# Performance work log

Measured on AMD Instinct MI355X. Metric: run time of the kernel, lower is better.

## Reference

```python
import jax, jax.numpy as jnp
import numpy as np

H, W = 32, 64          # img_size
NB = 4                 # fno_blocks
SCALE = 0.02


def setup_inputs() -> dict:
    key = jax.random.key(0)
    ks = jax.random.split(key, 8)
    B, N, C = 16, H * W, 768
    BS = C // NB
    x = jax.random.normal(ks[0], (B, N, C), dtype=jnp.float32)
    w1 = SCALE * jax.random.normal(ks[1], (2, NB, BS, BS), dtype=jnp.float32)
    b1 = SCALE * jax.random.normal(ks[2], (2, NB, BS), dtype=jnp.float32)
    w2 = SCALE * jax.random.normal(ks[3], (2, NB, BS, BS), dtype=jnp.float32)
    b2 = SCALE * jax.random.normal(ks[4], (2, NB, BS), dtype=jnp.float32)
    # Conv1d(C, C, kernel_size=1) == per-token linear layer over channels
    bias_w = jax.random.normal(ks[5], (C, C), dtype=jnp.float32) / np.sqrt(C)
    bias_b = jax.random.normal(ks[6], (C,), dtype=jnp.float32) * 0.01
    return {"x": x, "w1": w1, "b1": b1, "w2": w2, "b2": b2,
            "bias_w": bias_w, "bias_b": bias_b}


def _mul(a, w):
    # block-diagonal matmul: a [..., NB, BS], w [NB, BS, BS]
    return jnp.einsum('...bd,bdk->...bk', a, w)


def reference(x, w1, b1, w2, b2, bias_w, bias_b):
    B, N, C = x.shape
    BS = C // NB
    # Conv1d kernel-size-1 bias path
    bias = x @ bias_w.T + bias_b
    # spatial FFT
    xf = jnp.fft.rfftn(x.reshape(B, H, W, C), axes=(1, 2), norm='ortho')
    xf = xf.reshape(B, H, W // 2 + 1, NB, BS)
    xr, xi = xf.real, xf.imag
    # layer 1 (complex block-diag matmul + bias, ReLU on real/imag separately)
    r1 = jax.nn.relu(_mul(xr, w1[0]) - _mul(xi, w1[1]) + b1[0])
    i1 = jax.nn.relu(_mul(xr, w1[1]) + _mul(xi, w1[0]) + b1[1])
    # layer 2 -- NOTE: imag part uses the *updated* real part, matching the
    # original torch code's in-place reassignment order.
    r2 = _mul(r1, w2[0]) - _mul(i1, w2[1]) + b2[0]
    i2 = _mul(r2, w2[1]) + _mul(i1, w2[0]) + b2[1]
    xc = jax.lax.complex(r2, i2).reshape(B, H, W // 2 + 1, C)
    out = jnp.fft.irfftn(xc, s=(H, W), axes=(1, 2), norm='ortho')
    return out.reshape(B, N, C) + bias
```

## Files before the change

kernel.cpp:

```cpp
#include <hip/hip_runtime.h>
#include <hip/hip_bf16.h>
#include <stdint.h>

#define BB 16
#define HH 32
#define WW 64
#define CC 768
#define W2C 33
#define ROWW (2*CC)

typedef __bf16 bf16x8 __attribute__((ext_vector_type(8)));
typedef float f32x4 __attribute__((ext_vector_type(4)));

__device__ __forceinline__ unsigned short f2bf(float f) {
  __hip_bfloat16 h = __float2bfloat16(f);
  return __builtin_bit_cast(unsigned short, h);
}
__device__ __forceinline__ float bf2f(unsigned short u) {
  union { unsigned int i; float f; } x;
  x.i = ((unsigned int)u) << 16;
  return x.f;
}

__device__ __forceinline__ void g2l16(const void* g, void* l) {
  __builtin_amdgcn_global_load_lds((const __attribute__((address_space(1))) unsigned int*)g,
                                   (__attribute__((address_space(3))) unsigned int*)l,
                                   16, 0, 0);
}

__device__ __host__ constexpr int brevc(int x, int bits) {
  int r = 0;
  for (int i = 0; i < bits; ++i) r |= ((x >> i) & 1) << (bits - 1 - i);
  return r;
}

constexpr double TPI = 6.283185307179586476925286766559;
constexpr double tsin_(double x) {
  double t = x, s = x, x2 = x * x;
  for (int i = 1; i < 14; ++i) { t *= -x2 / (double)((2 * i) * (2 * i + 1)); s += t; }
  return s;
}
constexpr double tcos_(double x) {
  double t = 1.0, s = 1.0, x2 = x * x;
  for (int i = 1; i < 14; ++i) { t *= -x2 / (double)((2 * i - 1) * (2 * i)); s += t; }
  return s;
}
struct Tw64 { float c[64]; float s[64]; };
constexpr Tw64 mk_tw() {
  Tw64 r{};
  for (int k = 0; k < 64; ++k) {
    int q = k >> 4, m = k & 15;
    double a = (TPI / 64.0) * m;
    double cq = tcos_(a), sq = tsin_(a);
    double c, s;
    if (q == 0)      { c =  cq; s =  sq; }
    else if (q == 1) { c = -sq; s =  cq; }
    else if (q == 2) { c = -cq; s = -sq; }
    else             { c =  sq; s = -cq; }
    r.c[k] = (float)c;
    r.s[k] = (float)(-s);
  }
  return r;
}
constexpr Tw64 TW = mk_tw();

template<int N, bool INV>
__device__ __forceinline__ void fft_reg(float2 (&v)[N]) {
  constexpr int LOG2N = (N == 64) ? 6 : 5;
#pragma unroll
  for (int s = 0; s < LOG2N; ++s) {
    const int len = N >> s;
    const int half = len >> 1;
    const int tstep = 64 / len;
#pragma unroll
    for (int i = 0; i < N; i += len) {
#pragma unroll
      for (int j = 0; j < half; ++j) {
        float2 u = v[i + j];
        float2 t = v[i + j + half];
        float sr = u.x + t.x, si = u.y + t.y;
        float dr = u.x - t.x, di = u.y - t.y;
        float wr = TW.c[j * tstep];
        float wi = INV ? -TW.s[j * tstep] : TW.s[j * tstep];
        v[i + j] = make_float2(sr, si);
        v[i + j + half] = make_float2(dr * wr - di * wi, dr * wi + di * wr);
      }
    }
  }
}

__global__ __launch_bounds__(128) void fft_fwd_w(const float* __restrict__ x,
                                                 ushort2* __restrict__ yw,
                                                 unsigned short* __restrict__ xb) {
  __shared__ __align__(16) float xs[32][128];
  const int t = threadIdx.x;
  const int bh = blockIdx.x;
  const int c0 = blockIdx.y * 128;
  const float* xrow = x + (size_t)bh * (WW * CC) + c0;
  unsigned short* xbrow = xb + (size_t)bh * (WW * CC) + c0;
  const int rg = t >> 5;
  const int lc = (t & 31) * 4;
  float2 v[32];
#pragma unroll
  for (int half = 0; half < 2; ++half) {
    if (half) __syncthreads();
#pragma unroll
    for (int it = 0; it < 8; ++it) {
      const int w = half * 32 + it * 4 + rg;
      float4 f = *(const float4*)(xrow + (size_t)w * CC + lc);
      *(float4*)&xs[it * 4 + rg][lc] = f;
      *(ushort4*)(xbrow + (size_t)w * CC + lc) =
          make_ushort4(f2bf(f.x), f2bf(f.y), f2bf(f.z), f2bf(f.w));
    }
    __syncthreads();
#pragma unroll
    for (int n = 0; n < 16; ++n)
      v[half * 16 + n] = make_float2(xs[2 * n][t], xs[2 * n + 1][t]);
  }
  fft_reg<32, false>(v);
  ushort2* yp = yw + (size_t)bh * (W2C * CC) + c0 + t;
  {
    float2 Z0 = v[0];
    yp[0] = make_ushort2(f2bf(Z0.x + Z0.y), f2bf(0.f));
    yp[(size_t)32 * CC] = make_ushort2(f2bf(Z0.x - Z0.y), f2bf(0.f));
  }
#pragma unroll
  for (int k = 1; k < 32; ++k) {
    float2 Zk = v[brevc(k, 5)];
    float2 Zm = v[brevc(32 - k, 5)];
    float Er = 0.5f * (Zk.x + Zm.x), Ei = 0.5f * (Zk.y - Zm.y);
    float Odr = 0.5f * (Zk.y + Zm.y), Odi = -0.5f * (Zk.x - Zm.x);
    float wx = TW.c[k], wy = TW.s[k];
    float Xr = Er + wx * Odr - wy * Odi;
    float Xi = Ei + wx * Odi + wy * Odr;
    yp[(size_t)k * CC] = make_ushort2(f2bf(Xr), f2bf(Xi));
  }
}

__global__ __launch_bounds__(256) void fft_fwd_h(const ushort2* __restrict__ yw,
                                                 unsigned short* __restrict__ xf) {
  const int bk = blockIdx.x;
  const int b = bk / W2C, kw = bk - b * W2C;
  const int c = blockIdx.y * 256 + threadIdx.x;
  const ushort2* yp = yw + ((size_t)b * HH * W2C + kw) * CC + c;
  float2 v[32];
#pragma unroll
  for (int h = 0; h < 32; ++h) {
    ushort2 u = yp[(size_t)h * (W2C * CC)];
    v[h] = make_float2(bf2f(u.x), bf2f(u.y));
  }
  fft_reg<32, false>(v);
  const int nb = c / 192, cc = c - nb * 192;
  unsigned short* xp = xf + (size_t)nb * 384 + cc;
  const float s = 0.022097086912079608f;
#pragma unroll
  for (int kh = 0; kh < 32; ++kh) {
    float2 z = v[brevc(kh, 5)];
    size_t m = ((size_t)b * HH + kh) * W2C + kw;
    xp[m * ROWW] = f2bf(z.x * s);
    xp[m * ROWW + 192] = f2bf(z.y * s);
  }
}

__global__ __launch_bounds__(256) void fft_inv_h(const unsigned short* __restrict__ r2,
                                                 ushort2* __restrict__ g) {
  const int bk = blockIdx.x;
  const int b = bk / W2C, kw = bk - b * W2C;
  const int c = blockIdx.y * 256 + threadIdx.x;
  const int nb = c / 192, cc = c - nb * 192;
  const unsigned short* rp = r2 + (size_t)nb * 384 + cc;
  float2 v[32];
#pragma unroll
  for (int kh = 0; kh < 32; ++kh) {
    size_t m = ((size_t)b * HH + kh) * W2C + kw;
    v[kh] = make_float2(bf2f(rp[m * ROWW]), bf2f(rp[m * ROWW + 192]));
  }
  fft_reg<32, true>(v);
  ushort2* gp = g + ((size_t)b * HH * W2C + kw) * CC + c;
#pragma unroll
  for (int h = 0; h < 32; ++h) {
    float2 z = v[brevc(h, 5)];
    gp[(size_t)h * (W2C * CC)] = make_ushort2(f2bf(z.x), f2bf(z.y));
  }
}

__global__ __launch_bounds__(128) void fft_inv_w(const ushort2* __restrict__ g,
                                                 const unsigned short* __restrict__ biasb,
                                                 float* __restrict__ out) {
  __shared__ __align__(16) float ys[32][128];
  const int t = threadIdx.x;
  const int bh = blockIdx.x;
  const int c0 = blockIdx.y * 128;
  const ushort2* gp = g + (size_t)bh * (W2C * CC) + c0 + t;
  float2 v[32];
  {
    float X0 = bf2f(gp[0].x);
    float X32 = bf2f(gp[(size_t)32 * CC].x);
    v[0] = make_float2(0.5f * (X0 + X32), 0.5f * (X0 - X32));
  }
#pragma unroll
  for (int k = 1; k < 32; ++k) {
    ushort2 uk = gp[(size_t)k * CC];
    ushort2 um = gp[(size_t)(32 - k) * CC];
    float2 Xk = make_float2(bf2f(uk.x), bf2f(uk.y));
    float2 Xm = make_float2(bf2f(um.x), bf2f(um.y));
    float Ar = 0.5f * (Xk.x + Xm.x), Ai = 0.5f * (Xk.y - Xm.y);
    float Dr = 0.5f * (Xk.x - Xm.x), Di = 0.5f * (Xk.y + Xm.y);
    float wx = TW.c[k], wy = TW.s[k];
    float Br = wx * Dr + wy * Di;
    float Bi = wx * Di - wy * Dr;
    v[k] = make_float2(Ar - Bi, Ai + Br);
  }
  fft_reg<32, true>(v);
  const float s2 = 0.04419417382415922f;
  float* orow = out + (size_t)bh * (WW * CC) + c0;
  const unsigned short* brow = biasb + (size_t)bh * (WW * CC) + c0;
  const int rg = t >> 5;
  const int lc = (t & 31) * 4;
#pragma unroll
  for (int half = 0; half < 2; ++half) {
    if (half) __syncthreads();
#pragma unroll
    for (int n = 0; n < 16; ++n) {
      float2 z = v[brevc(half * 16 + n, 5)];
      ys[2 * n][t] = z.x * s2;
      ys[2 * n + 1][t] = z.y * s2;
    }
    __syncthreads();
#pragma unroll
    for (int it = 0; it < 8; ++it) {
      const int w = half * 32 + it * 4 + rg;
      float4 f = *(const float4*)&ys[it * 4 + rg][lc];
      ushort4 b4 = *(const ushort4*)(brow + (size_t)w * CC + lc);
      f.x += bf2f(b4.x); f.y += bf2f(b4.y); f.z += bf2f(b4.z); f.w += bf2f(b4.w);
      *(float4*)(orow + (size_t)w * CC + lc) = f;
    }
  }
}

template<bool RELU, bool OBF>
__global__ __launch_bounds__(256) void gemm_bt(
    const unsigned short* __restrict__ A, int lda, int aZ,
    const unsigned short* __restrict__ Bw, int K, int bZ,
    const float* __restrict__ bias, int biasZ,
    void* __restrict__ outp, int ldo, int oZ) {
  __shared__ __align__(16) unsigned short As[128 * 32];
  __shared__ __align__(16) unsigned short Bs[128 * 32];
  const int t = threadIdx.x;
  const int z = blockIdx.z;
  const size_t m0 = (size_t)blockIdx.x * 128;
  const int n0 = blockIdx.y * 128;
  const unsigned short* Ap = A + m0 * lda + (size_t)z * aZ;
  const unsigned short* Bp = Bw + (size_t)n0 * K + (size_t)z * bZ;
  const int lane = t & 63, wave = t >> 6;
  const int lr = lane & 15, quad = lane >> 4;
  const int wm = (wave >> 1) * 64, wn = (wave & 1) * 64;
  const int row = t >> 2;
  const int sl = t & 3;
  const int kb = (sl ^ ((row >> 1) & 3)) * 8;
  const int swzf = (lr >> 1) & 3;
  f32x4 acc[4][4] = {};
  for (int k0 = 0; k0 < K; k0 += 32) {
    const unsigned short* ga = Ap + (size_t)row * lda + (k0 + kb);
    g2l16(ga, &As[row * 32 + sl * 8]);
    g2l16(ga + (size_t)64 * lda, &As[(row + 64) * 32 + sl * 8]);
    const unsigned short* gb = Bp + (size_t)row * K + (k0 + kb);
    g2l16(gb, &Bs[row * 32 + sl * 8]);
    g2l16(gb + (size_t)64 * K, &Bs[(row + 64) * 32 + sl * 8]);
    __syncthreads();
    bf16x8 af[4], bfr[4];
#pragma unroll
    for (int mi = 0; mi < 4; ++mi)
      af[mi] = *(const bf16x8*)&As[(wm + mi * 16 + lr) * 32 + ((quad ^ swzf) * 8)];
#pragma unroll
    for (int ni = 0; ni < 4; ++ni)
      bfr[ni] = *(const bf16x8*)&Bs[(wn + ni * 16 + lr) * 32 + ((quad ^ swzf) * 8)];
#pragma unroll
    for (int mi = 0; mi < 4; ++mi)
#pragma unroll
      for (int ni = 0; ni < 4; ++ni)
        acc[mi][ni] = __builtin_amdgcn_mfma_f32_16x16x32_bf16(af[mi], bfr[ni], acc[mi][ni], 0, 0, 0);
    __syncthreads();
  }
#pragma unroll
  for (int mi = 0; mi < 4; ++mi) {
    const size_t mrow = m0 + wm + mi * 16 + quad * 4;
#pragma unroll
    for (int ni = 0; ni < 4; ++ni) {
      const int ncol = n0 + wn + ni * 16 + lr;
      const float bv = bias[z * biasZ + ncol];
#pragma unroll
      for (int r = 0; r < 4; ++r) {
        float vv = acc[mi][ni][r] + bv;
        if (RELU) vv = fmaxf(vv, 0.f);
        const size_t off = (mrow + r) * (size_t)ldo + (size_t)z * oZ + ncol;
        if (OBF) ((unsigned short*)outp)[off] = f2bf(vv);
        else ((float*)outp)[off] = vv;
      }
    }
  }
}

__global__ __launch_bounds__(256) void cvt_bf16(const float* __restrict__ in,
                                                unsigned short* __restrict__ outp) {
  const size_t i = ((size_t)blockIdx.x * 256 + threadIdx.x) * 4;
  float4 v = *(const float4*)(in + i);
  ushort4 o = make_ushort4(f2bf(v.x), f2bf(v.y), f2bf(v.z), f2bf(v.w));
  *(ushort4*)(outp + i) = o;
}

__global__ __launch_bounds__(256) void build_w1(const float* __restrict__ w1,
                                                const float* __restrict__ b1,
                                                unsigned short* __restrict__ w1t,
                                                float* __restrict__ bias1) {
  const int idx = blockIdx.x * 256 + threadIdx.x;
  const int nb = idx / (384 * 384);
  const int rem = idx - nb * (384 * 384);
  const int n = rem / 384, k = rem - (rem / 384) * 384;
  const bool khi = k >= 192, nhi = n >= 192;
  const int kk = khi ? k - 192 : k, nn = nhi ? n - 192 : n;
  float val;
  if (!khi && !nhi)      val =  w1[((0 * 4 + nb) * 192 + kk) * 192 + nn];
  else if (khi && !nhi)  val = -w1[((1 * 4 + nb) * 192 + kk) * 192 + nn];
  else if (!khi && nhi)  val =  w1[((1 * 4 + nb) * 192 + kk) * 192 + nn];
  else                   val =  w1[((0 * 4 + nb) * 192 + kk) * 192 + nn];
  w1t[((size_t)nb * 384 + n) * 384 + k] = f2bf(val);
  if (k == 0)
    bias1[nb * 384 + n] = nhi ? b1[(1 * 4 + nb) * 192 + nn] : b1[(0 * 4 + nb) * 192 + nn];
}

__global__ __launch_bounds__(256) void build_w2(const float* __restrict__ w2,
                                                const float* __restrict__ b2,
                                                unsigned short* __restrict__ w2t,
                                                float* __restrict__ bias2) {
  const int idx = blockIdx.x * 256 + threadIdx.x;
  const int nb = idx / (384 * 384);
  const int rem = idx - nb * (384 * 384);
  const int n = rem / 384, k = rem - (rem / 384) * 384;
  const bool khi = k >= 192, nhi = n >= 192;
  const int kk = khi ? k - 192 : k, nn = nhi ? n - 192 : n;
  float val;
  if (!khi && !nhi) {
    val = w2[((0 * 4 + nb) * 192 + kk) * 192 + nn];
  } else if (khi && !nhi) {
    val = -w2[((1 * 4 + nb) * 192 + kk) * 192 + nn];
  } else if (!khi && nhi) {
    float s = 0.f;
    for (int d = 0; d < 192; ++d)
      s += w2[((0 * 4 + nb) * 192 + kk) * 192 + d] * w2[((1 * 4 + nb) * 192 + d) * 192 + nn];
    val = s;
  } else {
    float s = 0.f;
    for (int d = 0; d < 192; ++d)
      s += w2[((1 * 4 + nb) * 192 + kk) * 192 + d] * w2[((1 * 4 + nb) * 192 + d) * 192 + nn];
    val = w2[((0 * 4 + nb) * 192 + kk) * 192 + nn] - s;
  }
  w2t[((size_t)nb * 384 + n) * 384 + k] = f2bf(val);
  if (k == 0) {
    float bv;
    if (!nhi) {
      bv = b2[(0 * 4 + nb) * 192 + nn];
    } else {
      float s = 0.f;
      for (int d = 0; d < 192; ++d)
        s += b2[(0 * 4 + nb) * 192 + d] * w2[((1 * 4 + nb) * 192 + d) * 192 + nn];
      bv = b2[(1 * 4 + nb) * 192 + nn] + s;
    }
    bias2[nb * 384 + n] = bv;
  }
}

extern "C" void kernel_launch(void* const* d_in, const int* in_sizes, int n_in,
                              void* d_out, int out_size, void* d_ws, size_t ws_size,
                              hipStream_t stream) {
  (void)in_sizes; (void)n_in; (void)out_size; (void)ws_size;
  const float* x  = (const float*)d_in[0];
  const float* w1 = (const float*)d_in[1];
  const float* b1 = (const float*)d_in[2];
  const float* w2 = (const float*)d_in[3];
  const float* b2 = (const float*)d_in[4];
  const float* bw = (const float*)d_in[5];
  const float* bb = (const float*)d_in[6];
  float* out = (float*)d_out;

  char* p = (char*)d_ws;
  unsigned short* buf1 = (unsigned short*)p; p += 51904512;
  unsigned short* buf2 = (unsigned short*)p; p += 51904512;
  unsigned short* buf3 = (unsigned short*)p; p += 51904512;
  unsigned short* bwb  = (unsigned short*)p; p += 1179648;
  unsigned short* w1t  = (unsigned short*)p; p += 1179648;
  unsigned short* w2t  = (unsigned short*)p; p += 1179648;
  float* bias1 = (float*)p; p += 6144;
  float* bias2 = (float*)p; p += 6144;

  cvt_bf16<<<589824 / 1024, 256, 0, stream>>>(bw, bwb);
  build_w1<<<589824 / 256, 256, 0, stream>>>(w1, b1, w1t, bias1);
  build_w2<<<589824 / 256, 256, 0, stream>>>(w2, b2, w2t, bias2);
  fft_fwd_w<<<dim3(BB * HH, 6), 128, 0, stream>>>(x, (ushort2*)buf1, buf2);
  fft_fwd_h<<<dim3(BB * W2C, 3), 256, 0, stream>>>((const ushort2*)buf1, buf3);
  gemm_bt<true, true><<<dim3(132, 3, 4), 256, 0, stream>>>(
      buf3, ROWW, 384, w1t, 384, 384 * 384, bias1, 384, buf1, ROWW, 384);
  gemm_bt<false, true><<<dim3(256, 6, 1), 256, 0, stream>>>(
      buf2, 768, 0, bwb, 768, 0, bb, 0, buf3, 768, 0);
  gemm_bt<false, true><<<dim3(132, 3, 4), 256, 0, stream>>>(
      buf1, ROWW, 384, w2t, 384, 384 * 384, bias2, 384, buf2, ROWW, 384);
  fft_inv_h<<<dim3(BB * W2C, 3), 256, 0, stream>>>(buf2, (ushort2*)buf1);
  fft_inv_w<<<dim3(BB * HH, 6), 128, 0, stream>>>((const ushort2*)buf1, buf3, out);
}
```

Before: 470.2 us.

## Pipeline GEMM loads with 4-stage LDS ring and wider bias-GEMM tiles

Replaces the single-buffered GEMM with a 4-stage shared-memory ring. Tiles are prefetched three steps ahead with explicit vmcnt waits and one barrier per k-step, so global loads overlap the MFMA work. It also raises wave priority around the MFMAs. The bias GEMM now uses 512-thread blocks with 128x256 tiles and an L2-friendly block-index swizzle. The cost is more LDS per block (up to 96 KB), which may cut occupancy, and hand-tuned wait counts that are fragile if the load count changes.

```diff
diff --git a/kernel.cpp b/kernel.cpp
--- a/kernel.cpp
+++ b/kernel.cpp
@@ -238,64 +238,89 @@
   }
 }
 
-template<bool RELU, bool OBF>
-__global__ __launch_bounds__(256) void gemm_bt(
+#define WAITVM(n) asm volatile("s_waitcnt vmcnt(" #n ")" ::: "memory")
+#define MEMFENCE() asm volatile("" ::: "memory")
+
+template<int WN, int BROWS, int NT, bool RELU>
+__global__ __launch_bounds__(128 * WN) void gemm_p(
     const unsigned short* __restrict__ A, int lda, int aZ,
-    const unsigned short* __restrict__ Bw, int K, int bZ,
+    const unsigned short* __restrict__ Bw, int ldb, int bZ,
     const float* __restrict__ bias, int biasZ,
-    void* __restrict__ outp, int ldo, int oZ) {
-  __shared__ __align__(16) unsigned short As[128 * 32];
-  __shared__ __align__(16) unsigned short Bs[128 * 32];
+    unsigned short* __restrict__ outp, int ldo, int oZ, int swzq) {
+  constexpr int BLOCK = 128 * WN;
+  constexpr int RPP = BLOCK / 4;
+  constexpr int PA = 128 / RPP;
+  constexpr int PB = BROWS / RPP;
+  constexpr int LT = PA + PB;
+  __shared__ __align__(16) unsigned short As[4][128 * 32];
+  __shared__ __align__(16) unsigned short Bs[4][BROWS * 32];
   const int t = threadIdx.x;
+  int bx = blockIdx.x;
+  if (swzq) bx = (bx & 7) * swzq + (bx >> 3);
   const int z = blockIdx.z;
-  const size_t m0 = (size_t)blockIdx.x * 128;
-  const int n0 = blockIdx.y * 128;
-  const unsigned short* Ap = A + m0 * lda + (size_t)z * aZ;
-  const unsigned short* Bp = Bw + (size_t)n0 * K + (size_t)z * bZ;
+  const size_t m0 = (size_t)bx * 128;
+  const int n0 = blockIdx.y * BROWS;
   const int lane = t & 63, wave = t >> 6;
   const int lr = lane & 15, quad = lane >> 4;
-  const int wm = (wave >> 1) * 64, wn = (wave & 1) * 64;
-  const int row = t >> 2;
-  const int sl = t & 3;
-  const int kb = (sl ^ ((row >> 1) & 3)) * 8;
-  const int swzf = (lr >> 1) & 3;
+  const int wmo = (wave / WN) * 64;
+  const int wno = (wave % WN) * 64;
+  const int srow = t >> 2, sl = t & 3;
+  const int kb = (sl ^ ((srow >> 1) & 3)) * 8;
+  const int coff = ((quad ^ ((lr >> 1) & 3)) * 8);
+  const unsigned short* Abase = A + (size_t)z * aZ + (m0 + srow) * (size_t)lda + kb;
+  const unsigned short* Bbase = Bw + (size_t)z * bZ + (size_t)(n0 + srow) * ldb + kb;
   f32x4 acc[4][4] = {};
-  for (int k0 = 0; k0 < K; k0 += 32) {
-    const unsigned short* ga = Ap + (size_t)row * lda + (k0 + kb);
-    g2l16(ga, &As[row * 32 + sl * 8]);
-    g2l16(ga + (size_t)64 * lda, &As[(row + 64) * 32 + sl * 8]);
-    const unsigned short* gb = Bp + (size_t)row * K + (k0 + kb);
-    g2l16(gb, &Bs[row * 32 + sl * 8]);
-    g2l16(gb + (size_t)64 * K, &Bs[(row + 64) * 32 + sl * 8]);
-    __syncthreads();
-    bf16x8 af[4], bfr[4];
+
+#define STG(tt_) do { \
+    const int s_ = (tt_) & 3; const int k0_ = (tt_) * 32; \
+    _Pragma("unroll") \
+    for (int p = 0; p < PA; ++p) \
+      g2l16(Abase + (size_t)(p * RPP) * lda + k0_, &As[s_][(srow + p * RPP) * 32 + sl * 8]); \
+    _Pragma("unroll") \
+    for (int p = 0; p < PB; ++p) \
+      g2l16(Bbase + (size_t)(p * RPP) * ldb + k0_, &Bs[s_][(srow + p * RPP) * 32 + sl * 8]); \
+  } while (0)
+
+  STG(0); STG(1); STG(2);
+  if constexpr (LT == 3) WAITVM(6); else WAITVM(8);
+  MEMFENCE(); __builtin_amdgcn_s_barrier(); MEMFENCE();
+
+  for (int tt = 0; tt < NT; ++tt) {
+    if (tt < NT - 3) STG(tt + 3);
+    const int s = tt & 3;
+    bf16x8 af[4], bfv[4];
 #pragma unroll
     for (int mi = 0; mi < 4; ++mi)
-      af[mi] = *(const bf16x8*)&As[(wm + mi * 16 + lr) * 32 + ((quad ^ swzf) * 8)];
+      af[mi] = *(const bf16x8*)&As[s][(wmo + mi * 16 + lr) * 32 + coff];
 #pragma unroll
     for (int ni = 0; ni < 4; ++ni)
-      bfr[ni] = *(const bf16x8*)&Bs[(wn + ni * 16 + lr) * 32 + ((quad ^ swzf) * 8)];
+      bfv[ni] = *(const bf16x8*)&Bs[s][(wno + ni * 16 + lr) * 32 + coff];
+    __builtin_amdgcn_s_setprio(1);
 #pragma unroll
     for (int mi = 0; mi < 4; ++mi)
 #pragma unroll
       for (int ni = 0; ni < 4; ++ni)
-        acc[mi][ni] = __builtin_amdgcn_mfma_f32_16x16x32_bf16(af[mi], bfr[ni], acc[mi][ni], 0, 0, 0);
-    __syncthreads();
-  }
+        acc[mi][ni] = __builtin_amdgcn_mfma_f32_16x16x32_bf16(af[mi], bfv[ni], acc[mi][ni], 0, 0, 0);
+    __builtin_amdgcn_s_setprio(0);
+    if (tt < NT - 3) { if constexpr (LT == 3) WAITVM(6); else WAITVM(8); }
+    else if (tt == NT - 3) { if constexpr (LT == 3) WAITVM(3); else WAITVM(4); }
+    else if (tt == NT - 2) WAITVM(0);
+    if (tt < NT - 1) { MEMFENCE(); __builtin_amdgcn_s_barrier(); MEMFENCE(); }
+  }
+#undef STG
+
 #pragma unroll
   for (int mi = 0; mi < 4; ++mi) {
-    const size_t mrow = m0 + wm + mi * 16 + quad * 4;
+    const size_t mrow = m0 + wmo + mi * 16 + quad * 4;
 #pragma unroll
     for (int ni = 0; ni < 4; ++ni) {
-      const int ncol = n0 + wn + ni * 16 + lr;
+      const int ncol = n0 + wno + ni * 16 + lr;
       const float bv = bias[z * biasZ + ncol];
 #pragma unroll
       for (int r = 0; r < 4; ++r) {
         float vv = acc[mi][ni][r] + bv;
         if (RELU) vv = fmaxf(vv, 0.f);
-        const size_t off = (mrow + r) * (size_t)ldo + (size_t)z * oZ + ncol;
-        if (OBF) ((unsigned short*)outp)[off] = f2bf(vv);
-        else ((float*)outp)[off] = vv;
+        outp[(mrow + r) * (size_t)ldo + (size_t)z * oZ + ncol] = f2bf(vv);
       }
     }
   }
@@ -398,12 +423,12 @@
   build_w2<<<589824 / 256, 256, 0, stream>>>(w2, b2, w2t, bias2);
   fft_fwd_w<<<dim3(BB * HH, 6), 128, 0, stream>>>(x, (ushort2*)buf1, buf2);
   fft_fwd_h<<<dim3(BB * W2C, 3), 256, 0, stream>>>((const ushort2*)buf1, buf3);
-  gemm_bt<true, true><<<dim3(132, 3, 4), 256, 0, stream>>>(
-      buf3, ROWW, 384, w1t, 384, 384 * 384, bias1, 384, buf1, ROWW, 384);
-  gemm_bt<false, true><<<dim3(256, 6, 1), 256, 0, stream>>>(
-      buf2, 768, 0, bwb, 768, 0, bb, 0, buf3, 768, 0);
-  gemm_bt<false, true><<<dim3(132, 3, 4), 256, 0, stream>>>(
-      buf1, ROWW, 384, w2t, 384, 384 * 384, bias2, 384, buf2, ROWW, 384);
+  gemm_p<2, 128, 12, true><<<dim3(132, 3, 4), 256, 0, stream>>>(
+      buf3, ROWW, 384, w1t, 384, 384 * 384, bias1, 384, buf1, ROWW, 384, 0);
+  gemm_p<4, 256, 24, false><<<dim3(256, 3, 1), 512, 0, stream>>>(
+      buf2, 768, 0, bwb, 768, 0, bb, 0, buf3, 768, 0, 32);
+  gemm_p<2, 128, 12, false><<<dim3(132, 3, 4), 256, 0, stream>>>(
+      buf1, ROWW, 384, w2t, 384, 384 * 384, bias2, 384, buf2, ROWW, 384, 0);
   fft_inv_h<<<dim3(BB * W2C, 3), 256, 0, stream>>>(buf2, (ushort2*)buf1);
   fft_inv_w<<<dim3(BB * HH, 6), 128, 0, stream>>>((const ushort2*)buf1, buf3, out);
 }
```

After: 500.4 us. 6.4% more time.
